# Kernel optimization log

Hardware: AMD Instinct MI355X
Metric: run time of the kernel (lower is better)

The kernel has to match this reference:

```python
import jax, jax.numpy as jnp
import numpy as np

B, T, E, H, DL, CC, K = 64, 2048, 512, 128, 1024, 32, 31


def setup_inputs() -> dict:
    key = jax.random.key(0)
    ks = jax.random.split(key, 8)
    return {
        "encoder_output": jax.random.normal(ks[0], (B, T, E), jnp.float32),
        "processed_encoder_output": jax.random.normal(ks[1], (B, T, H), jnp.float32),
        "lstm_output": jax.random.normal(ks[2], (B, 1, DL), jnp.float32),
        "attention_weights_cum": jax.random.uniform(ks[3], (B, T), jnp.float32),
        # learned params (torch Linear stores [out, in]; y = x @ W.T)
        "W_lstm": jax.random.normal(ks[4], (H, DL), jnp.float32) * 0.02,
        "conv_w": jax.random.normal(ks[5], (CC, 1, K), jnp.float32) * 0.1,
        "W_loc": jax.random.normal(ks[6], (H, CC), jnp.float32) * 0.1,
        "W_e": jax.random.normal(ks[7], (1, H), jnp.float32) * 0.1,
    }


def _forward(encoder_output, processed_encoder_output, lstm_output,
             attention_weights_cum, W_lstm, conv_w, W_loc, W_e):
    # [B,1,1024] @ [1024,128] -> [B,1,128]
    processed_lstm = jnp.einsum('bqd,hd->bqh', lstm_output, W_lstm)
    # location conv: [B,1,T] -> [B,32,T], same padding
    loc = lax.conv_general_dilated(
        attention_weights_cum[:, None, :], conv_w,
        window_strides=(1,), padding=[(K // 2, K // 2)],
        dimension_numbers=('NCH', 'OIH', 'NCH'))
    # transpose to [B,T,32] then dense to [B,T,128]
    processed_attn = jnp.einsum('bct,hc->bth', loc, W_loc)
    # additive energies: [B,T,128] -> [B,T]
    energies = jnp.einsum('bth,oh->bto',
                          jnp.tanh(processed_lstm + processed_attn + processed_encoder_output),
                          W_e)[..., 0]
    attention_weights = jax.nn.softmax(energies, axis=1)  # [B,T]
    # bmm: [B,1,T] @ [B,T,E] -> [B,1,E]
    attention_context = jnp.einsum('bt,bte->be', attention_weights, encoder_output)[:, None, :]
    return attention_context, attention_weights

from jax import lax


def reference(encoder_output, processed_encoder_output, lstm_output,
              attention_weights_cum, W_lstm, conv_w, W_loc, W_e):
    return _forward(encoder_output, processed_encoder_output, lstm_output,
                    attention_weights_cum, W_lstm, conv_w, W_loc, W_e)
```

## Files before the change

### kernel.cpp

```cpp
#include <hip/hip_runtime.h>
#include <math.h>


#define BB 64
#define TT 2048
#define EE 512
#define HH 128
#define DLL 1024
#define CCC 32
#define KK 31

#define WS_FW   0
#define WS_PL   4096
#define WS_EN   12288
#define WS_ST   143360
#define WS_PART 144384

__global__ __launch_bounds__(256) void k0_prep(const float* __restrict__ lstm,
                                               const float* __restrict__ Wl,
                                               const float* __restrict__ cw,
                                               const float* __restrict__ Wloc,
                                               float* __restrict__ ws) {
  const int blk = blockIdx.x;
  const int tid = threadIdx.x;
  if (blk < 2048) {
    const int wave = tid >> 6, lane = tid & 63;
    const int wg = blk * 4 + wave;
    const int b = wg >> 7, h = wg & 127;
    const float4* wr = (const float4*)(Wl + (size_t)h * DLL);
    const float4* lr = (const float4*)(lstm + (size_t)b * DLL);
    float s = 0.f;
#pragma unroll
    for (int m = 0; m < 4; ++m) {
      float4 a = wr[m * 64 + lane];
      float4 c = lr[m * 64 + lane];
      s += a.x * c.x + a.y * c.y + a.z * c.z + a.w * c.w;
    }
#pragma unroll
    for (int m = 1; m < 64; m <<= 1) s += __shfl_xor(s, m, 64);
    if (lane == 0) ws[WS_PL + b * HH + h] = s;
  } else {
    __shared__ __align__(16) float wl_s[HH * CCC];
    __shared__ __align__(16) float cw_s[CCC * KK];
#pragma unroll
    for (int m = 0; m < 4; ++m)
      ((float4*)wl_s)[tid + 256 * m] = ((const float4*)Wloc)[tid + 256 * m];
    if (tid < 248) ((float4*)cw_s)[tid] = ((const float4*)cw)[tid];
    __syncthreads();
    const int h = tid >> 1;
    const int kbase = (tid & 1) * 16;
    const int kn = (tid & 1) ? 15 : 16;
    for (int kk = 0; kk < kn; ++kk) {
      const int k = kbase + kk;
      float s = 0.f;
#pragma unroll
      for (int c = 0; c < CCC; ++c) s += wl_s[h * CCC + c] * cw_s[c * KK + k];
      ws[WS_FW + h * 32 + k] = s;
    }
    if (tid & 1) ws[WS_FW + h * 32 + 31] = 0.f;
  }
}

__global__ __launch_bounds__(512, 4) void k1_fused(const float* __restrict__ pe,
                                                   const float* __restrict__ aw,
                                                   const float* __restrict__ We,
                                                   const float* __restrict__ enc,
                                                   float* __restrict__ ws) {
  const int b = blockIdx.y;
  const int chunk = blockIdx.x;
  const int t0 = chunk * 256;
  const int tid = threadIdx.x;
  const int wave = tid >> 6, lane = tid & 63;

  __shared__ __align__(16) float fw_s[HH * 32];
  __shared__ __align__(16) float aw_s[288];
  __shared__ float pl_s[128];
  __shared__ float we_s[128];
  __shared__ float w_s[256];
  __shared__ __align__(16) float4 acc_s[128];
  __shared__ float m_arr[4], s_arr[4];
  __shared__ int flag_s[4];

  {
    const float4* src = (const float4*)(ws + WS_FW);
    float4* dst = (float4*)fw_s;
    dst[tid] = src[tid];
    dst[tid + 512] = src[tid + 512];
  }
  if (tid < 288) {
    const int tg = t0 - 16 + tid;
    aw_s[tid] = (tg >= 0 && tg < TT) ? aw[b * TT + tg] : 0.f;
  }
  if (tid < 128) {
    pl_s[tid] = ws[WS_PL + b * HH + tid];
    we_s[tid] = We[tid];
  }
  if (tid < 4) flag_s[tid] = 0;
  __syncthreads();

  if (wave < 4) {
    const int lt = wave * 64 + lane;
    float wreg[32];
#pragma unroll
    for (int k = 0; k < 32; ++k) wreg[k] = aw_s[lt + 1 + k];
    const float4* pr4 = (const float4*)(pe + ((size_t)b * TT + t0 + lt) * HH);
    float e_acc = 0.f;
#pragma unroll 1
    for (int h0 = 0; h0 < 128; h0 += 16) {
      float4 ptv[4];
#pragma unroll
      for (int i = 0; i < 4; ++i) ptv[i] = pr4[(h0 >> 2) + i];
      float pts[16];
#pragma unroll
      for (int i = 0; i < 4; ++i) {
        pts[4 * i + 0] = ptv[i].x; pts[4 * i + 1] = ptv[i].y;
        pts[4 * i + 2] = ptv[i].z; pts[4 * i + 3] = ptv[i].w;
      }
#pragma unroll 2
      for (int hh = 0; hh < 16; ++hh) {
        const int h = h0 + hh;
        const float4* fr = (const float4*)&fw_s[h * 32];
        float a0 = pl_s[h] + pts[hh];
        float a1 = 0.f;
#pragma unroll
        for (int q = 0; q < 8; ++q) {
          const float4 f = fr[q];
          a0 = fmaf(f.x, wreg[4 * q + 0], a0);
          a1 = fmaf(f.y, wreg[4 * q + 1], a1);
          a0 = fmaf(f.z, wreg[4 * q + 2], a0);
          a1 = fmaf(f.w, wreg[4 * q + 3], a1);
        }
        const float x = a0 + a1;
        const float th = 1.f - 2.f / (__expf(2.f * x) + 1.f);
        e_acc = fmaf(we_s[h], th, e_acc);
      }
    }
    ws[WS_EN + b * TT + t0 + lt] = e_acc;

    float m = e_acc;
#pragma unroll
    for (int s = 1; s < 64; s <<= 1) m = fmaxf(m, __shfl_xor(m, s, 64));
    float p = __expf(e_acc - m);
#pragma unroll
    for (int s = 1; s < 64; s <<= 1) p += __shfl_xor(p, s, 64);
    w_s[lt] = __expf(e_acc - m);
    if (lane == 0) { m_arr[wave] = m; s_arr[wave] = p; }
    __hip_atomic_store(&flag_s[wave], 1, __ATOMIC_RELEASE,
                       __HIP_MEMORY_SCOPE_WORKGROUP);
  } else {
    const int cid = tid - 256;
    const int c4 = cid & 127;
    const int tp = cid >> 7;
    const float4* enc4 = (const float4*)(enc + ((size_t)b * TT + t0) * EE);
    float4 a0 = {0.f, 0.f, 0.f, 0.f}, a1 = {0.f, 0.f, 0.f, 0.f};
    float mrun = -3.4e38f;
#pragma unroll 1
    for (int sub = 0; sub < 4; ++sub) {
      while (!__hip_atomic_load(&flag_s[sub], __ATOMIC_ACQUIRE,
                                __HIP_MEMORY_SCOPE_WORKGROUP))
        __builtin_amdgcn_s_sleep(2);
      const float mi = m_arr[sub];
      const float mnew = fmaxf(mrun, mi);
      const float so = __expf(mrun - mnew);
      const float sc = __expf(mi - mnew);
      a0.x *= so; a0.y *= so; a0.z *= so; a0.w *= so;
      a1.x *= so; a1.y *= so; a1.z *= so; a1.w *= so;
      const float* wp = &w_s[sub * 64];
#pragma unroll 8
      for (int i = 0; i < 32; ++i) {
        const int t = 2 * i + tp;
        const float w = wp[t] * sc;
        const float4 v = enc4[(size_t)(sub * 64 + t) * 128 + c4];
        if (i & 1) {
          a1.x = fmaf(w, v.x, a1.x); a1.y = fmaf(w, v.y, a1.y);
          a1.z = fmaf(w, v.z, a1.z); a1.w = fmaf(w, v.w, a1.w);
        } else {
          a0.x = fmaf(w, v.x, a0.x); a0.y = fmaf(w, v.y, a0.y);
          a0.z = fmaf(w, v.z, a0.z); a0.w = fmaf(w, v.w, a0.w);
        }
      }
      mrun = mnew;
    }
    a0.x += a1.x; a0.y += a1.y; a0.z += a1.z; a0.w += a1.w;
    if (tp == 1) acc_s[c4] = a0;
    else {
      acc_s[c4].x = acc_s[c4].x;
    }
    __syncthreads();
    if (tp == 0) {
      const float4 o = acc_s[c4];
      a0.x += o.x; a0.y += o.y; a0.z += o.z; a0.w += o.w;
      ((float4*)(ws + WS_PART))[(size_t)(b * 8 + chunk) * 128 + c4] = a0;
    }
    if (cid == 0) {
      const float mb = fmaxf(fmaxf(m_arr[0], m_arr[1]),
                             fmaxf(m_arr[2], m_arr[3]));
      float sb = 0.f;
#pragma unroll
      for (int c = 0; c < 4; ++c) sb += s_arr[c] * __expf(m_arr[c] - mb);
      float* st = ws + WS_ST + (b * 8 + chunk) * 2;
      st[0] = mb;
      st[1] = sb;
    }
    return;
  }
  __syncthreads();
}

__global__ __launch_bounds__(256) void k2_combine(const float* __restrict__ ws,
                                                  float* __restrict__ wts,
                                                  float* __restrict__ ctx) {
  const int b = blockIdx.x;
  const int tid = threadIdx.x;

  const float* st = ws + WS_ST + b * 16;
  float mb = -3.4e38f;
#pragma unroll
  for (int c = 0; c < 8; ++c) mb = fmaxf(mb, st[2 * c]);
  float S = 0.f;
#pragma unroll
  for (int c = 0; c < 8; ++c) S += st[2 * c + 1] * __expf(st[2 * c] - mb);
  const float inv = 1.f / S;

  __shared__ float esc[8];
  if (tid < 8) esc[tid] = __expf(st[2 * tid] - mb) * inv;
  __syncthreads();

  const float4* en4 = (const float4*)(ws + WS_EN + (size_t)b * TT);
  float4* w4 = (float4*)(wts + (size_t)b * TT);
#pragma unroll
  for (int j = 0; j < 2; ++j) {
    const float4 e = en4[tid * 2 + j];
    float4 w;
    w.x = __expf(e.x - mb) * inv;
    w.y = __expf(e.y - mb) * inv;
    w.z = __expf(e.z - mb) * inv;
    w.w = __expf(e.w - mb) * inv;
    w4[tid * 2 + j] = w;
  }

  const float2* p2 = (const float2*)(ws + WS_PART) + (size_t)b * 8 * 256 + tid;
  float2 s = {0.f, 0.f};
#pragma unroll
  for (int c = 0; c < 8; ++c) {
    const float2 v = p2[c * 256];
    s.x = fmaf(esc[c], v.x, s.x);
    s.y = fmaf(esc[c], v.y, s.y);
  }
  ((float2*)ctx)[b * 256 + tid] = s;
}

extern "C" void kernel_launch(void* const* d_in, const int* in_sizes, int n_in,
                              void* d_out, int out_size, void* d_ws, size_t ws_size,
                              hipStream_t stream) {
  const float* enc  = (const float*)d_in[0];
  const float* pe   = (const float*)d_in[1];
  const float* lstm = (const float*)d_in[2];
  const float* awc  = (const float*)d_in[3];
  const float* Wl   = (const float*)d_in[4];
  const float* cw   = (const float*)d_in[5];
  const float* Wloc = (const float*)d_in[6];
  const float* We   = (const float*)d_in[7];

  float* out = (float*)d_out;
  float* ctx = out;
  float* wts = out + BB * EE;
  float* ws = (float*)d_ws;

  k0_prep<<<2049, 256, 0, stream>>>(lstm, Wl, cw, Wloc, ws);
  k1_fused<<<dim3(8, BB), 512, 0, stream>>>(pe, awc, We, enc, ws);
  k2_combine<<<BB, 256, 0, stream>>>(ws, wts, ctx);
}
```

Before: 86.97 us.

## Split energy computation across waves by hidden dim so sub-chunks finish in order

The energy waves now each own a 32-wide slice of the hidden dimension and loop over the four 64-timestep sub-chunks, writing partial sums to shared memory. The last wave to finish a sub-chunk, detected with an atomic counter, reduces the partials, computes softmax stats and raises that sub-chunk's flag. This lets the context waves start on sub-chunk 0 earlier instead of waiting on one wave per sub-chunk, improving overlap between the energy and context phases. It adds shared-memory traffic, atomics and a different fw_s access pattern, and the __syncthreads placement is now split across divergent branches.

```diff
diff --git a/kernel.cpp b/kernel.cpp
--- a/kernel.cpp
+++ b/kernel.cpp
@@ -76,10 +76,11 @@
   __shared__ __align__(16) float aw_s[288];
   __shared__ float pl_s[128];
   __shared__ float we_s[128];
+  __shared__ __align__(16) float pp[4][4][64];
   __shared__ float w_s[256];
   __shared__ __align__(16) float4 acc_s[128];
   __shared__ float m_arr[4], s_arr[4];
-  __shared__ int flag_s[4];
+  __shared__ int flag_s[4], cnt_s[4];
 
   {
     const float4* src = (const float4*)(ws + WS_FW);
@@ -95,30 +96,32 @@
     pl_s[tid] = ws[WS_PL + b * HH + tid];
     we_s[tid] = We[tid];
   }
-  if (tid < 4) flag_s[tid] = 0;
+  if (tid < 4) { flag_s[tid] = 0; cnt_s[tid] = 0; }
   __syncthreads();
 
   if (wave < 4) {
-    const int lt = wave * 64 + lane;
-    float wreg[32];
-#pragma unroll
-    for (int k = 0; k < 32; ++k) wreg[k] = aw_s[lt + 1 + k];
-    const float4* pr4 = (const float4*)(pe + ((size_t)b * TT + t0 + lt) * HH);
-    float e_acc = 0.f;
+    const int hbase = wave * 32;
 #pragma unroll 1
-    for (int h0 = 0; h0 < 128; h0 += 16) {
-      float4 ptv[4];
-#pragma unroll
-      for (int i = 0; i < 4; ++i) ptv[i] = pr4[(h0 >> 2) + i];
-      float pts[16];
-#pragma unroll
-      for (int i = 0; i < 4; ++i) {
+    for (int sub = 0; sub < 4; ++sub) {
+      const int lt = sub * 64 + lane;
+      float wreg[32];
+#pragma unroll
+      for (int k = 0; k < 32; ++k) wreg[k] = aw_s[lt + 1 + k];
+      const float4* pr4 = (const float4*)(pe + ((size_t)b * TT + t0 + lt) * HH) +
+                          (hbase >> 2);
+      float4 ptv[8];
+#pragma unroll
+      for (int i = 0; i < 8; ++i) ptv[i] = pr4[i];
+      float pts[32];
+#pragma unroll
+      for (int i = 0; i < 8; ++i) {
         pts[4 * i + 0] = ptv[i].x; pts[4 * i + 1] = ptv[i].y;
         pts[4 * i + 2] = ptv[i].z; pts[4 * i + 3] = ptv[i].w;
       }
+      float partial = 0.f;
 #pragma unroll 2
-      for (int hh = 0; hh < 16; ++hh) {
-        const int h = h0 + hh;
+      for (int hh = 0; hh < 32; ++hh) {
+        const int h = hbase + hh;
         const float4* fr = (const float4*)&fw_s[h * 32];
         float a0 = pl_s[h] + pts[hh];
         float a1 = 0.f;
@@ -132,21 +135,32 @@
         }
         const float x = a0 + a1;
         const float th = 1.f - 2.f / (__expf(2.f * x) + 1.f);
-        e_acc = fmaf(we_s[h], th, e_acc);
-      }
-    }
-    ws[WS_EN + b * TT + t0 + lt] = e_acc;
-
-    float m = e_acc;
-#pragma unroll
-    for (int s = 1; s < 64; s <<= 1) m = fmaxf(m, __shfl_xor(m, s, 64));
-    float p = __expf(e_acc - m);
-#pragma unroll
-    for (int s = 1; s < 64; s <<= 1) p += __shfl_xor(p, s, 64);
-    w_s[lt] = __expf(e_acc - m);
-    if (lane == 0) { m_arr[wave] = m; s_arr[wave] = p; }
-    __hip_atomic_store(&flag_s[wave], 1, __ATOMIC_RELEASE,
-                       __HIP_MEMORY_SCOPE_WORKGROUP);
+        partial = fmaf(we_s[h], th, partial);
+      }
+      pp[sub][wave][lane] = partial;
+
+      int old = 0;
+      if (lane == 0)
+        old = __hip_atomic_fetch_add(&cnt_s[sub], 1, __ATOMIC_ACQ_REL,
+                                     __HIP_MEMORY_SCOPE_WORKGROUP);
+      old = __shfl(old, 0, 64);
+      if (old == 3) {
+        const float e = pp[sub][0][lane] + pp[sub][1][lane] +
+                        pp[sub][2][lane] + pp[sub][3][lane];
+        ws[WS_EN + b * TT + t0 + lt] = e;
+        float m = e;
+#pragma unroll
+        for (int s = 1; s < 64; s <<= 1) m = fmaxf(m, __shfl_xor(m, s, 64));
+        float p = __expf(e - m);
+#pragma unroll
+        for (int s = 1; s < 64; s <<= 1) p += __shfl_xor(p, s, 64);
+        w_s[lt] = __expf(e - m);
+        if (lane == 0) { m_arr[sub] = m; s_arr[sub] = p; }
+        __hip_atomic_store(&flag_s[sub], 1, __ATOMIC_RELEASE,
+                           __HIP_MEMORY_SCOPE_WORKGROUP);
+      }
+    }
+    __syncthreads();
   } else {
     const int cid = tid - 256;
     const int c4 = cid & 127;
@@ -183,9 +197,6 @@
     }
     a0.x += a1.x; a0.y += a1.y; a0.z += a1.z; a0.w += a1.w;
     if (tp == 1) acc_s[c4] = a0;
-    else {
-      acc_s[c4].x = acc_s[c4].x;
-    }
     __syncthreads();
     if (tp == 0) {
       const float4 o = acc_s[c4];
@@ -202,9 +213,7 @@
       st[0] = mb;
       st[1] = sb;
     }
-    return;
-  }
-  __syncthreads();
+  }
 }
 
 __global__ __launch_bounds__(256) void k2_combine(const float* __restrict__ ws,
```

Measured after the change: 78.29 us. 10.0% less time.
